# Performance work log

Hardware: AMD Instinct MI355X
Metric: run time of the kernel (lower is better)

The kernel has to match this reference:

```python
import jax, jax.numpy as jnp
import numpy as np

D_MODEL = 1024
H = 16
D_K = D_MODEL // H


def setup_inputs() -> dict:
    key = jax.random.key(0)
    ks = jax.random.split(key, 12)
    B, S = 2, 2048
    inp = {
        "q": jax.random.normal(ks[0], (B, S, D_MODEL), jnp.float32),
        "k": jax.random.normal(ks[1], (B, S, D_MODEL), jnp.float32),
        "v": jax.random.normal(ks[2], (B, S, D_MODEL), jnp.float32),
        "mask": jax.random.randint(ks[3], (1, 1, S, S), 0, 2, jnp.int32),
    }
    s = 1.0 / np.sqrt(D_MODEL)
    inp["wq_w"] = jax.random.normal(ks[4], (D_MODEL, D_MODEL), jnp.float32) * s
    inp["wq_b"] = jnp.zeros((D_MODEL,), jnp.float32)
    inp["wk_w"] = jax.random.normal(ks[5], (D_MODEL, D_MODEL), jnp.float32) * s
    inp["wk_b"] = jnp.zeros((D_MODEL,), jnp.float32)
    inp["wv_w"] = jax.random.normal(ks[6], (D_MODEL, D_MODEL), jnp.float32) * s
    inp["wv_b"] = jnp.zeros((D_MODEL,), jnp.float32)
    inp["wo_w"] = jax.random.normal(ks[7], (D_MODEL, D_MODEL), jnp.float32) * s
    inp["wo_b"] = jnp.zeros((D_MODEL,), jnp.float32)
    return inp


def reference(q, k, v, mask, wq_w, wq_b, wk_w, wk_b, wv_w, wv_b, wo_w, wo_b):
    B, S, _ = q.shape
    # projections (torch Linear: x @ W^T + b)
    def proj(x, w, b):
        y = x @ w.T + b
        return y.reshape(B, S, H, D_K).transpose(0, 2, 1, 3)  # [B,H,S,Dk]

    Q = proj(q, wq_w, wq_b)
    K = proj(k, wk_w, wk_b)
    V = proj(v, wv_w, wv_b)

    scores = jnp.einsum("bhqd,bhkd->bhqk", Q, K) / jnp.sqrt(jnp.float32(D_K))
    # source quirk: masked positions set to 1e-9 (NOT -inf) before softmax
    scores = jnp.where(mask == 0, jnp.float32(1e-9), scores)
    attn = jax.nn.softmax(scores, axis=-1)
    out = jnp.einsum("bhqk,bhkd->bhqd", attn, V)
    out = out.transpose(0, 2, 1, 3).reshape(B, S, H * D_K)
    return out @ wo_w.T + wo_b
```

## Files before the change

kernel.cpp:

```cpp
#include <hip/hip_runtime.h>

typedef _Float16 half_t;
typedef _Float16 h8 __attribute__((ext_vector_type(8)));
typedef _Float16 h4 __attribute__((ext_vector_type(4)));
typedef _Float16 h2 __attribute__((ext_vector_type(2)));
typedef float f32x4 __attribute__((ext_vector_type(4)));
typedef float f32x16 __attribute__((ext_vector_type(16)));

#define S_LEN 2048
#define DMODEL 1024
#define NHEAD 16
#define HDK 64
#define NB 2
#define MROWS (NB * S_LEN)
#define LOG2E 1.44269504089f

__device__ __forceinline__ void gload_lds16(const void* g, void* l) {
  __builtin_amdgcn_global_load_lds(
      (const __attribute__((address_space(1))) unsigned int*)g,
      (__attribute__((address_space(3))) unsigned int*)l, 16, 0, 0);
}

__device__ __forceinline__ float fast_exp2(float x) {
  float r;
  asm("v_exp_f32 %0, %1" : "=v"(r) : "v"(x));
  return r;
}

__device__ __forceinline__ int swz(int row, int colByte) {
  return row * 128 + (colByte ^ ((row & 7) << 4));
}

__global__ __launch_bounds__(256) void pre_kernel(
    const float* __restrict__ wq, const float* __restrict__ wk,
    const float* __restrict__ wv, const float* __restrict__ wo,
    const int* __restrict__ mask,
    half_t* Wq, half_t* Wk, half_t* Wv, half_t* Wo,
    unsigned int* mbits) {
  const int gid = blockIdx.x, tid = threadIdx.x;
  if (gid < 4096) {
    int i = gid * 256 + tid;
    int rgn = i >> 18, off = i & 262143;
    const float* src = rgn == 0 ? wq : rgn == 1 ? wk : rgn == 2 ? wv : wo;
    half_t* dst = rgn == 0 ? Wq : rgn == 1 ? Wk : rgn == 2 ? Wv : Wo;
    float4 vv = ((const float4*)src)[off];
    h4 o;
    o[0] = (half_t)vv.x; o[1] = (half_t)vv.y; o[2] = (half_t)vv.z; o[3] = (half_t)vv.w;
    ((h4*)dst)[off] = o;
  } else {
    int i = (gid - 4096) * 256 + tid;
    int mv = mask[i];
    unsigned long long bm = __ballot(mv != 0);
    int lane = tid & 63;
    if (lane == 0)       mbits[i >> 5] = (unsigned int)bm;
    else if (lane == 32) mbits[i >> 5] = (unsigned int)(bm >> 32);
  }
}

template <int EPI>
__global__ __launch_bounds__(256) void gemm_kernel(
    const void* A0, const void* A1, const void* A2,
    const half_t* __restrict__ W0, const half_t* __restrict__ W1, const half_t* __restrict__ W2,
    const float* __restrict__ b0, const float* __restrict__ b1, const float* __restrict__ b2,
    void* o0, void* o1, void* o2) {
  const void* A; const half_t* W; const float* bias; void* out; float scale;
  if (blockIdx.z == 0)      { A = A0; W = W0; bias = b0; out = o0; scale = (EPI == 0) ? 0.125f * LOG2E : 1.0f; }
  else if (blockIdx.z == 1) { A = A1; W = W1; bias = b1; out = o1; scale = 1.0f; }
  else                      { A = A2; W = W2; bias = b2; out = o2; scale = 1.0f; }

  __shared__ half_t As[128 * 32];
  __shared__ half_t Bs[128 * 32];
  const int tid = threadIdx.x;
  const int w = tid >> 6, lane = tid & 63;
  const int wm = w >> 1, wn = w & 1;
  const int bm = blockIdx.x, bn = blockIdx.y;
  const int crow = lane >> 2;
  const int ck = (lane & 3) * 8;

  f32x4 acc[4][4] = {};

  const float* Af0 = (const float*)A + (size_t)(bm * 128 + w * 16 + crow) * DMODEL + ck;
  const float* Af1 = Af0 + 64 * DMODEL;
  const half_t* Ah0 = (const half_t*)A + (size_t)(bm * 128 + w * 16 + crow) * DMODEL + ck;
  const half_t* Ah1 = Ah0 + 64 * DMODEL;
  const half_t* Wg0 = W + (size_t)(bn * 128 + w * 16 + crow) * DMODEL + ck;
  const half_t* Wg1 = Wg0 + 64 * DMODEL;
  half_t* lA0 = As + w * 512;
  half_t* lA1 = As + (w + 4) * 512;
  half_t* lB0 = Bs + w * 512;
  half_t* lB1 = Bs + (w + 4) * 512;

  for (int kt = 0; kt < DMODEL; kt += 32) {
    __syncthreads();
    gload_lds16(Wg0 + kt, lB0);
    gload_lds16(Wg1 + kt, lB1);
    if (EPI == 0) {
      float4 x0 = *(const float4*)(Af0 + kt);
      float4 x1 = *(const float4*)(Af0 + kt + 4);
      float4 y0 = *(const float4*)(Af1 + kt);
      float4 y1 = *(const float4*)(Af1 + kt + 4);
      h8 ha, hb;
      ha[0] = (half_t)x0.x; ha[1] = (half_t)x0.y; ha[2] = (half_t)x0.z; ha[3] = (half_t)x0.w;
      ha[4] = (half_t)x1.x; ha[5] = (half_t)x1.y; ha[6] = (half_t)x1.z; ha[7] = (half_t)x1.w;
      hb[0] = (half_t)y0.x; hb[1] = (half_t)y0.y; hb[2] = (half_t)y0.z; hb[3] = (half_t)y0.w;
      hb[4] = (half_t)y1.x; hb[5] = (half_t)y1.y; hb[6] = (half_t)y1.z; hb[7] = (half_t)y1.w;
      *(h8*)((char*)lA0 + (size_t)lane * 16) = ha;
      *(h8*)((char*)lA1 + (size_t)lane * 16) = hb;
    } else {
      gload_lds16(Ah0 + kt, lA0);
      gload_lds16(Ah1 + kt, lA1);
    }
    __syncthreads();

    h8 af[4], bf[4];
    const int rr = lane & 15;
    const int kk = (lane >> 4) * 8;
#pragma unroll
    for (int i = 0; i < 4; ++i)
      af[i] = *(const h8*)(As + (wm * 64 + i * 16 + rr) * 32 + kk);
#pragma unroll
    for (int j = 0; j < 4; ++j)
      bf[j] = *(const h8*)(Bs + (wn * 64 + j * 16 + rr) * 32 + kk);
#pragma unroll
    for (int i = 0; i < 4; ++i)
#pragma unroll
      for (int j = 0; j < 4; ++j)
        acc[i][j] = __builtin_amdgcn_mfma_f32_16x16x32_f16(af[i], bf[j], acc[i][j], 0, 0, 0);
  }

  const int r0 = bm * 128 + wm * 64;
  const int c0 = bn * 128 + wn * 64;
#pragma unroll
  for (int j = 0; j < 4; ++j) {
    int col = c0 + j * 16 + (lane & 15);
    float bc = bias[col];
#pragma unroll
    for (int i = 0; i < 4; ++i) {
#pragma unroll
      for (int jj = 0; jj < 4; ++jj) {
        int row = r0 + i * 16 + (lane >> 4) * 4 + jj;
        float val = acc[i][j][jj] + bc;
        if (EPI == 0) {
          int bb = row >> 11, s = row & (S_LEN - 1);
          int hh = col >> 6, dk = col & 63;
          if (blockIdx.z == 2) {
            ((half_t*)out)[((size_t)((bb * NHEAD + hh) * HDK + dk)) * S_LEN + s] = (half_t)val;
          } else {
            ((half_t*)out)[(((size_t)(bb * NHEAD + hh)) * S_LEN + s) * HDK + dk] =
                (half_t)(val * scale);
          }
        } else {
          ((float*)out)[(size_t)row * DMODEL + col] = val;
        }
      }
    }
  }
}

__global__ __launch_bounds__(256, 4) void attn_kernel(
    const half_t* __restrict__ Qp, const half_t* __restrict__ Kp,
    const half_t* __restrict__ VTp, const unsigned int* __restrict__ mbits,
    half_t* __restrict__ AO) {
  __shared__ char smem[32768];

  const int tid = threadIdx.x, w = tid >> 6, lane = tid & 63;
  const int qg = w >> 1, kh = w & 1;
  const int id = blockIdx.x;
  const int xcd = id & 7, rest = id >> 3;
  const int bh = (xcd << 2) | (rest >> 5);
  const int qt = rest & 31;
  const int b = bh >> 4, h = bh & 15;
  const int q32 = lane & 31, hi = lane >> 5;
  const int qbase = qt * 64 + qg * 32;
  const half_t* Qb = Qp + (size_t)bh * (S_LEN * HDK);
  const char* Kb = (const char*)(Kp + (size_t)bh * (S_LEN * HDK));
  const char* VTb = (const char*)(VTp + (size_t)bh * (S_LEN * HDK));
  const unsigned int* mrow = mbits + (size_t)(qbase + q32) * (S_LEN / 32);

  char* Ks = smem;
  char* Vs = smem + 16384;
  const int srow = w * 16 + (lane >> 3);
  const int scb = (lane & 7) * 16;

  h8 qf[4];
#pragma unroll
  for (int s = 0; s < 4; ++s)
    qf[s] = *(const h8*)(Qb + (size_t)(qbase + q32) * HDK + s * 16 + hi * 8);

  f32x16 acc0 = {}, acc1 = {};
  float l_run = 0.f;

  unsigned int mw = mrow[kh];
#pragma unroll
  for (int p = 0; p < 2; ++p) {
    int r = srow + p * 8;
    gload_lds16(Kb + (size_t)r * 128 + (scb ^ ((r & 7) << 4)),
                Ks + (w * 16 + p * 8) * 128);
    gload_lds16(VTb + (size_t)r * (S_LEN * 2) + (scb ^ ((r & 7) << 4)),
                Vs + (w * 16 + p * 8) * 128);
  }
  __syncthreads();

  int cur = 0;
  for (int t = 0; t < 32; ++t) {
    const unsigned int mwc = mw >> (hi * 4);

    if (t < 31) {
      const int kvn = t + 1;
#pragma unroll
      for (int p = 0; p < 2; ++p) {
        int r = srow + p * 8;
        gload_lds16(Kb + (size_t)(kvn * 64 + r) * 128 + (scb ^ ((r & 7) << 4)),
                    Ks + (cur ^ 1) * 8192 + (w * 16 + p * 8) * 128);
        gload_lds16(VTb + (size_t)r * (S_LEN * 2) + kvn * 128 + (scb ^ ((r & 7) << 4)),
                    Vs + (cur ^ 1) * 8192 + (w * 16 + p * 8) * 128);
      }
      mw = mrow[kvn * 2 + kh];
    }

    const char* kb = Ks + cur * 8192;
    const char* vb = Vs + cur * 8192;
    f32x16 sc = {};
    __builtin_amdgcn_s_setprio(1);
#pragma unroll
    for (int s = 0; s < 4; ++s) {
      h8 kf = *(const h8*)(kb + swz(kh * 32 + q32, s * 32 + hi * 16));
      sc = __builtin_amdgcn_mfma_f32_32x32x16_f16(kf, qf[s], sc, 0, 0, 0);
    }
    __builtin_amdgcn_s_setprio(0);

    h8 vf00 = *(const h8*)(vb + swz(q32, kh * 64 + hi * 16));
    h8 vf01 = *(const h8*)(vb + swz(q32, kh * 64 + 32 + hi * 16));
    h8 vf10 = *(const h8*)(vb + swz(32 + q32, kh * 64 + hi * 16));
    h8 vf11 = *(const h8*)(vb + swz(32 + q32, kh * 64 + 32 + hi * 16));

#pragma unroll
    for (int rg = 0; rg < 16; ++rg) {
      const int bit = (rg & 3) + 8 * (rg >> 2);
      float p = fast_exp2(((mwc >> bit) & 1u) ? sc[rg] : 0.0f);
      sc[rg] = p;
      l_run += p;
    }

    h8 pb[2];
#pragma unroll
    for (int s = 0; s < 2; ++s) {
      const int rb = s * 8;
      union { h2 h; unsigned int u; } c01, c23, c45, c67;
      c01.h[0] = (half_t)sc[rb + 0]; c01.h[1] = (half_t)sc[rb + 1];
      c23.h[0] = (half_t)sc[rb + 2]; c23.h[1] = (half_t)sc[rb + 3];
      c45.h[0] = (half_t)sc[rb + 4]; c45.h[1] = (half_t)sc[rb + 5];
      c67.h[0] = (half_t)sc[rb + 6]; c67.h[1] = (half_t)sc[rb + 7];
      auto rA = __builtin_amdgcn_permlane32_swap(c01.u, c45.u, false, false);
      auto rB = __builtin_amdgcn_permlane32_swap(c23.u, c67.u, false, false);
      union { unsigned int u[4]; h8 v; } bw;
      bw.u[0] = rA[0]; bw.u[1] = rB[0]; bw.u[2] = rA[1]; bw.u[3] = rB[1];
      pb[s] = bw.v;
    }

    __builtin_amdgcn_s_setprio(1);
    acc0 = __builtin_amdgcn_mfma_f32_32x32x16_f16(vf00, pb[0], acc0, 0, 0, 0);
    acc1 = __builtin_amdgcn_mfma_f32_32x32x16_f16(vf10, pb[0], acc1, 0, 0, 0);
    acc0 = __builtin_amdgcn_mfma_f32_32x32x16_f16(vf01, pb[1], acc0, 0, 0, 0);
    acc1 = __builtin_amdgcn_mfma_f32_32x32x16_f16(vf11, pb[1], acc1, 0, 0, 0);
    __builtin_amdgcn_s_setprio(0);

    __syncthreads();
    cur ^= 1;
  }

  float* my = (float*)smem + (qg * 64 + lane) * 33;
  if (kh) {
#pragma unroll
    for (int rg = 0; rg < 16; ++rg) { my[rg] = acc0[rg]; my[16 + rg] = acc1[rg]; }
    my[32] = l_run;
  }
  __syncthreads();
  if (!kh) {
#pragma unroll
    for (int rg = 0; rg < 16; ++rg) { acc0[rg] += my[rg]; acc1[rg] += my[16 + rg]; }
    l_run += my[32];
    l_run += __shfl_xor(l_run, 32);

    const float inv = 1.0f / l_run;
    const int qrow = qbase + q32;
    half_t* aob = AO + (size_t)(b * S_LEN + qrow) * DMODEL + h * HDK;
#pragma unroll
    for (int rq = 0; rq < 4; ++rq) {
      h4 s0, s1;
#pragma unroll
      for (int j = 0; j < 4; ++j) {
        s0[j] = (half_t)(acc0[rq * 4 + j] * inv);
        s1[j] = (half_t)(acc1[rq * 4 + j] * inv);
      }
      const int d0 = 8 * rq + 4 * hi;
      *(h4*)(aob + d0) = s0;
      *(h4*)(aob + 32 + d0) = s1;
    }
  }
}

extern "C" void kernel_launch(void* const* d_in, const int* in_sizes, int n_in,
                              void* d_out, int out_size, void* d_ws, size_t ws_size,
                              hipStream_t stream) {
  const float* q    = (const float*)d_in[0];
  const float* k    = (const float*)d_in[1];
  const float* v    = (const float*)d_in[2];
  const int*   mask = (const int*)d_in[3];
  const float* wq_w = (const float*)d_in[4];
  const float* wq_b = (const float*)d_in[5];
  const float* wk_w = (const float*)d_in[6];
  const float* wk_b = (const float*)d_in[7];
  const float* wv_w = (const float*)d_in[8];
  const float* wv_b = (const float*)d_in[9];
  const float* wo_w = (const float*)d_in[10];
  const float* wo_b = (const float*)d_in[11];
  float* out = (float*)d_out;

  char* ws = (char*)d_ws;
  const size_t MB = (size_t)1 << 20;
  half_t* AO = (half_t*)(ws + 0 * MB);
  half_t* Wq = (half_t*)(ws + 24 * MB);
  half_t* Wk = (half_t*)(ws + 26 * MB);
  half_t* Wv = (half_t*)(ws + 28 * MB);
  half_t* Wo = (half_t*)(ws + 30 * MB);
  half_t* Qp = (half_t*)(ws + 32 * MB);
  half_t* Kp = (half_t*)(ws + 40 * MB);
  half_t* VT = (half_t*)(ws + 48 * MB);
  unsigned int* mbits = (unsigned int*)(ws + 56 * MB);

  pre_kernel<<<20480, 256, 0, stream>>>(wq_w, wk_w, wv_w, wo_w, mask,
                                        Wq, Wk, Wv, Wo, mbits);
  gemm_kernel<0><<<dim3(32, 8, 3), 256, 0, stream>>>(
      q, k, v, Wq, Wk, Wv, wq_b, wk_b, wv_b, (void*)Qp, (void*)Kp, (void*)VT);
  attn_kernel<<<1024, 256, 0, stream>>>(Qp, Kp, VT, mbits, AO);
  gemm_kernel<1><<<dim3(32, 8, 1), 256, 0, stream>>>(
      AO, AO, AO, Wo, Wo, Wo, wo_b, wo_b, wo_b, (void*)out, (void*)out, (void*)out);

  (void)in_sizes; (void)n_in; (void)out_size; (void)ws_size;
}
```

Measured before the change: 142.1 us.

## Pre-convert activations to fp16 and widen GEMM K-tile with swizzled LDS

The q/k/v fp32 activations are now converted to fp16 in the pre-kernel, so the projection GEMM can load A tiles straight into LDS with direct global-to-LDS loads instead of converting in registers. The GEMM K-tile grows from 32 to 64 halves, with an XOR swizzle on the LDS layout to avoid bank conflicts, which halves the number of barrier pairs per tile. The cost is an extra round trip through global memory for the fp16 activations, plus a larger pre-kernel grid.

```diff
diff --git a/kernel.cpp b/kernel.cpp
--- a/kernel.cpp
+++ b/kernel.cpp
@@ -32,23 +32,33 @@
 }
 
 __global__ __launch_bounds__(256) void pre_kernel(
+    const float* __restrict__ q, const float* __restrict__ k, const float* __restrict__ v,
     const float* __restrict__ wq, const float* __restrict__ wk,
     const float* __restrict__ wv, const float* __restrict__ wo,
     const int* __restrict__ mask,
+    half_t* Xq, half_t* Xk, half_t* Xv,
     half_t* Wq, half_t* Wk, half_t* Wv, half_t* Wo,
     unsigned int* mbits) {
   const int gid = blockIdx.x, tid = threadIdx.x;
-  if (gid < 4096) {
+  if (gid < 16384) {
     int i = gid * 256 + tid;
-    int rgn = i >> 18, off = i & 262143;
-    const float* src = rgn == 0 ? wq : rgn == 1 ? wk : rgn == 2 ? wv : wo;
-    half_t* dst = rgn == 0 ? Wq : rgn == 1 ? Wk : rgn == 2 ? Wv : Wo;
+    const float* src; half_t* dst; int off;
+    if (i < 3145728) {
+      int rgn = i >> 20; off = i & 1048575;
+      src = rgn == 0 ? q : rgn == 1 ? k : v;
+      dst = rgn == 0 ? Xq : rgn == 1 ? Xk : Xv;
+    } else {
+      int j = i - 3145728;
+      int rgn = j >> 18; off = j & 262143;
+      src = rgn == 0 ? wq : rgn == 1 ? wk : rgn == 2 ? wv : wo;
+      dst = rgn == 0 ? Wq : rgn == 1 ? Wk : rgn == 2 ? Wv : Wo;
+    }
     float4 vv = ((const float4*)src)[off];
     h4 o;
     o[0] = (half_t)vv.x; o[1] = (half_t)vv.y; o[2] = (half_t)vv.z; o[3] = (half_t)vv.w;
     ((h4*)dst)[off] = o;
   } else {
-    int i = (gid - 4096) * 256 + tid;
+    int i = (gid - 16384) * 256 + tid;
     int mv = mask[i];
     unsigned long long bm = __ballot(mv != 0);
     int lane = tid & 63;
@@ -59,73 +69,61 @@
 
 template <int EPI>
 __global__ __launch_bounds__(256) void gemm_kernel(
-    const void* A0, const void* A1, const void* A2,
+    const half_t* __restrict__ A0, const half_t* __restrict__ A1, const half_t* __restrict__ A2,
     const half_t* __restrict__ W0, const half_t* __restrict__ W1, const half_t* __restrict__ W2,
     const float* __restrict__ b0, const float* __restrict__ b1, const float* __restrict__ b2,
     void* o0, void* o1, void* o2) {
-  const void* A; const half_t* W; const float* bias; void* out; float scale;
+  const half_t* A; const half_t* W; const float* bias; void* out; float scale;
   if (blockIdx.z == 0)      { A = A0; W = W0; bias = b0; out = o0; scale = (EPI == 0) ? 0.125f * LOG2E : 1.0f; }
   else if (blockIdx.z == 1) { A = A1; W = W1; bias = b1; out = o1; scale = 1.0f; }
   else                      { A = A2; W = W2; bias = b2; out = o2; scale = 1.0f; }
 
-  __shared__ half_t As[128 * 32];
-  __shared__ half_t Bs[128 * 32];
+  __shared__ half_t As[128 * 64];
+  __shared__ half_t Bs[128 * 64];
   const int tid = threadIdx.x;
   const int w = tid >> 6, lane = tid & 63;
   const int wm = w >> 1, wn = w & 1;
   const int bm = blockIdx.x, bn = blockIdx.y;
-  const int crow = lane >> 2;
-  const int ck = (lane & 3) * 8;
 
   f32x4 acc[4][4] = {};
 
-  const float* Af0 = (const float*)A + (size_t)(bm * 128 + w * 16 + crow) * DMODEL + ck;
-  const float* Af1 = Af0 + 64 * DMODEL;
-  const half_t* Ah0 = (const half_t*)A + (size_t)(bm * 128 + w * 16 + crow) * DMODEL + ck;
-  const half_t* Ah1 = Ah0 + 64 * DMODEL;
-  const half_t* Wg0 = W + (size_t)(bn * 128 + w * 16 + crow) * DMODEL + ck;
-  const half_t* Wg1 = Wg0 + 64 * DMODEL;
-  half_t* lA0 = As + w * 512;
-  half_t* lA1 = As + (w + 4) * 512;
-  half_t* lB0 = Bs + w * 512;
-  half_t* lB1 = Bs + (w + 4) * 512;
-
-  for (int kt = 0; kt < DMODEL; kt += 32) {
+  const int r8 = lane >> 3;
+  const int scb2 = ((lane & 7) * 16) ^ (r8 << 4);
+  const char* Ab = (const char*)A + (size_t)(bm * 128) * 2048;
+  const char* Wb = (const char*)W + (size_t)(bn * 128) * 2048;
+  char* AsB = (char*)As;
+  char* BsB = (char*)Bs;
+
+  const int rr = lane & 15;
+  const int kgB = (lane >> 4) * 16;
+  const int swzr = (rr & 7) << 4;
+
+  for (int kb0 = 0; kb0 < 2048; kb0 += 128) {
     __syncthreads();
-    gload_lds16(Wg0 + kt, lB0);
-    gload_lds16(Wg1 + kt, lB1);
-    if (EPI == 0) {
-      float4 x0 = *(const float4*)(Af0 + kt);
-      float4 x1 = *(const float4*)(Af0 + kt + 4);
-      float4 y0 = *(const float4*)(Af1 + kt);
-      float4 y1 = *(const float4*)(Af1 + kt + 4);
-      h8 ha, hb;
-      ha[0] = (half_t)x0.x; ha[1] = (half_t)x0.y; ha[2] = (half_t)x0.z; ha[3] = (half_t)x0.w;
-      ha[4] = (half_t)x1.x; ha[5] = (half_t)x1.y; ha[6] = (half_t)x1.z; ha[7] = (half_t)x1.w;
-      hb[0] = (half_t)y0.x; hb[1] = (half_t)y0.y; hb[2] = (half_t)y0.z; hb[3] = (half_t)y0.w;
-      hb[4] = (half_t)y1.x; hb[5] = (half_t)y1.y; hb[6] = (half_t)y1.z; hb[7] = (half_t)y1.w;
-      *(h8*)((char*)lA0 + (size_t)lane * 16) = ha;
-      *(h8*)((char*)lA1 + (size_t)lane * 16) = hb;
-    } else {
-      gload_lds16(Ah0 + kt, lA0);
-      gload_lds16(Ah1 + kt, lA1);
+#pragma unroll
+    for (int p = 0; p < 4; ++p) {
+      const int row = p * 32 + w * 8 + r8;
+      const size_t srow = (size_t)row * 2048 + kb0 + scb2;
+      gload_lds16(Ab + srow, AsB + (p * 32 + w * 8) * 128);
+      gload_lds16(Wb + srow, BsB + (p * 32 + w * 8) * 128);
     }
     __syncthreads();
 
-    h8 af[4], bf[4];
-    const int rr = lane & 15;
-    const int kk = (lane >> 4) * 8;
-#pragma unroll
-    for (int i = 0; i < 4; ++i)
-      af[i] = *(const h8*)(As + (wm * 64 + i * 16 + rr) * 32 + kk);
-#pragma unroll
-    for (int j = 0; j < 4; ++j)
-      bf[j] = *(const h8*)(Bs + (wn * 64 + j * 16 + rr) * 32 + kk);
-#pragma unroll
-    for (int i = 0; i < 4; ++i)
-#pragma unroll
-      for (int j = 0; j < 4; ++j)
-        acc[i][j] = __builtin_amdgcn_mfma_f32_16x16x32_f16(af[i], bf[j], acc[i][j], 0, 0, 0);
+#pragma unroll
+    for (int h = 0; h < 2; ++h) {
+      const int kcb = (kgB + h * 64) ^ swzr;
+      h8 af[4], bf[4];
+#pragma unroll
+      for (int i = 0; i < 4; ++i) {
+        af[i] = *(const h8*)(AsB + (wm * 64 + i * 16 + rr) * 128 + kcb);
+        bf[i] = *(const h8*)(BsB + (wn * 64 + i * 16 + rr) * 128 + kcb);
+      }
+#pragma unroll
+      for (int i = 0; i < 4; ++i)
+#pragma unroll
+        for (int j = 0; j < 4; ++j)
+          acc[i][j] = __builtin_amdgcn_mfma_f32_16x16x32_f16(af[i], bf[j], acc[i][j], 0, 0, 0);
+    }
   }
 
   const int r0 = bm * 128 + wm * 64;
@@ -319,7 +317,9 @@
 
   char* ws = (char*)d_ws;
   const size_t MB = (size_t)1 << 20;
-  half_t* AO = (half_t*)(ws + 0 * MB);
+  half_t* Xq = (half_t*)(ws + 0 * MB);
+  half_t* Xk = (half_t*)(ws + 8 * MB);
+  half_t* Xv = (half_t*)(ws + 16 * MB);
   half_t* Wq = (half_t*)(ws + 24 * MB);
   half_t* Wk = (half_t*)(ws + 26 * MB);
   half_t* Wv = (half_t*)(ws + 28 * MB);
@@ -328,11 +328,12 @@
   half_t* Kp = (half_t*)(ws + 40 * MB);
   half_t* VT = (half_t*)(ws + 48 * MB);
   unsigned int* mbits = (unsigned int*)(ws + 56 * MB);
-
-  pre_kernel<<<20480, 256, 0, stream>>>(wq_w, wk_w, wv_w, wo_w, mask,
-                                        Wq, Wk, Wv, Wo, mbits);
+  half_t* AO = Xq;
+
+  pre_kernel<<<32768, 256, 0, stream>>>(q, k, v, wq_w, wk_w, wv_w, wo_w, mask,
+                                        Xq, Xk, Xv, Wq, Wk, Wv, Wo, mbits);
   gemm_kernel<0><<<dim3(32, 8, 3), 256, 0, stream>>>(
-      q, k, v, Wq, Wk, Wv, wq_b, wk_b, wv_b, (void*)Qp, (void*)Kp, (void*)VT);
+      Xq, Xk, Xv, Wq, Wk, Wv, wq_b, wk_b, wv_b, (void*)Qp, (void*)Kp, (void*)VT);
   attn_kernel<<<1024, 256, 0, stream>>>(Qp, Kp, VT, mbits, AO);
   gemm_kernel<1><<<dim3(32, 8, 1), 256, 0, stream>>>(
       AO, AO, AO, Wo, Wo, Wo, wo_b, wo_b, wo_b, (void*)out, (void*)out, (void*)out);
```

After: 156.7 us. 1.1x slower.
